# Optimization experiments

Measured on AMD Instinct MI355X. Metric: run time of the kernel, lower is better.

The kernel has to match this reference:

```python
import math
import jax, jax.numpy as jnp
import numpy as np

B, FEAT, H, W = 4, 256, 48, 48
NH = 8
PE = 10            # pe_dim -> 3*PE = 30 positional channels
DK = FEAT // NH    # 32
DV = FEAT // NH    # 32
SCALE = 2.0 * math.pi
TEMPERATURE = 10000.0
BN_EPS = 1e-5


def pos_en_sine(h, w, num_pos_feats=PE):
    """3-axis sine positional encoding (y, x, and a constant 'o' axis) -> [3*PE, h, w]."""
    eps = 1e-6
    ones = jnp.ones((h, w), jnp.float32)
    y_embed = jnp.cumsum(ones, axis=0)
    x_embed = jnp.cumsum(ones, axis=1)
    y_embed = y_embed / (y_embed[-1:, :] + eps) * SCALE
    x_embed = x_embed / (x_embed[:, -1:] + eps) * SCALE
    o_embed = ones * SCALE  # third axis, constant when no explicit pos is given
    dim_t = jnp.arange(num_pos_feats, dtype=jnp.float32)
    dim_t = TEMPERATURE ** (2.0 * jnp.floor(dim_t / 2.0) / num_pos_feats)

    def enc(e):  # e: [h, w] -> [h, w, PE] interleaved sin/cos
        p = e[..., None] / dim_t
        return jnp.stack([jnp.sin(p[..., 0::2]), jnp.cos(p[..., 1::2])], axis=-1).reshape(h, w, num_pos_feats)

    pe = jnp.concatenate([enc(y_embed), enc(x_embed), enc(o_embed)], axis=-1)  # [h, w, 3*PE]
    return jnp.transpose(pe, (2, 0, 1))  # [3*PE, h, w]


def conv1x1(w, x):  # w: [out_c, in_c], x: [b, in_c, h, w]
    return jnp.einsum('oc,bchw->bohw', w, x)


def setup_inputs() -> dict:
    key = jax.random.key(0)
    ks = jax.random.split(key, 16)
    s = 0.02
    return {
        'q': jax.random.normal(ks[0], (B, FEAT, H, W), jnp.float32),
        'k': jax.random.normal(ks[1], (B, FEAT, H, W), jnp.float32),
        'v': jax.random.normal(ks[2], (B, FEAT, H, W), jnp.float32),
        'wq': jax.random.normal(ks[3], (NH * DK, FEAT + 3 * PE), jnp.float32) * s,
        'wk': jax.random.normal(ks[4], (NH * DK, FEAT + 3 * PE), jnp.float32) * s,
        'wv': jax.random.normal(ks[5], (NH * DV, FEAT), jnp.float32) * s,
        'wfc': jax.random.normal(ks[6], (FEAT, NH * DV), jnp.float32) * s,
        'w1': jax.random.normal(ks[7], (FEAT, FEAT), jnp.float32) * s,
        'b1': jnp.zeros((FEAT,), jnp.float32),
        'w2': jax.random.normal(ks[8], (FEAT, FEAT), jnp.float32) * s,
        'b2': jnp.zeros((FEAT,), jnp.float32),
        'gamma': jnp.ones((FEAT,), jnp.float32),
        'beta': jnp.zeros((FEAT,), jnp.float32),
    }


def reference(q, k, v, wq, wk, wv, wfc, w1, b1, w2, b2, gamma, beta):
    b, c, h, w = q.shape
    n = h * w
    pe = pos_en_sine(h, w)                                # [3*PE, h, w]
    peb = jnp.broadcast_to(pe[None], (b,) + pe.shape)
    qc = jnp.concatenate([q, peb], axis=1)                # [b, FEAT+30, h, w]
    kc = jnp.concatenate([k, peb], axis=1)
    # multi-head softmax attention over all spatial tokens
    Q = conv1x1(wq, qc).reshape(b, NH, DK, n)             # [b, nh, dk, n]
    K = conv1x1(wk, kc).reshape(b, NH, DK, n)
    V = conv1x1(wv, v).reshape(b, NH, DV, n)
    scores = jnp.einsum('bhdn,bhdm->bhnm', Q, K) / jnp.sqrt(jnp.float32(DK))
    attn = jax.nn.softmax(scores, axis=-1)                # [b, nh, n, n]
    O = jnp.einsum('bhnm,bhdm->bhdn', attn, V).reshape(b, NH * DV, h, w)
    O = conv1x1(wfc, O)                                   # [b, FEAT, h, w]
    # pointwise FFN + residual
    h1 = jax.nn.relu(conv1x1(w1, O) + b1[None, :, None, None])
    h2 = conv1x1(w2, h1) + b2[None, :, None, None]
    out = O + h2
    # BatchNorm2d (training mode: batch statistics over (b, h, w), biased var)
    mean = jnp.mean(out, axis=(0, 2, 3), keepdims=True)
    var = jnp.var(out, axis=(0, 2, 3), keepdims=True)
    out = (out - mean) / jnp.sqrt(var + BN_EPS)
    out = out * gamma[None, :, None, None] + beta[None, :, None, None]
    return out
```

## Files before the change

kernel.cpp:

```cpp
#include <hip/hip_runtime.h>
#include <hip/hip_bf16.h>

#define NTOK 2304

typedef short  short8  __attribute__((ext_vector_type(8)));
typedef unsigned short ushort8v __attribute__((ext_vector_type(8)));
typedef float  f32x4   __attribute__((ext_vector_type(4)));

static __device__ __forceinline__ unsigned short f2bfu(float f){
  __hip_bfloat16 h = __float2bfloat16(f);
  union { __hip_bfloat16 h; unsigned short u; } cv; cv.h = h; return cv.u;
}

static __device__ __forceinline__ void plane32(unsigned &a, unsigned &b){
  asm("v_permlane32_swap_b32 %0, %1" : "+v"(a), "+v"(b));
}
static __device__ __forceinline__ void plane16(unsigned &a, unsigned &b){
  asm("v_permlane16_swap_b32 %0, %1" : "+v"(a), "+v"(b));
}
static __device__ __forceinline__ short8 xpose_p(f32x4 sa, f32x4 sb){
  unsigned x0, x1, y0, y1;
  asm("v_cvt_pk_bf16_f32 %0, %1, %2" : "=v"(x0) : "v"(sa[0]), "v"(sa[1]));
  asm("v_cvt_pk_bf16_f32 %0, %1, %2" : "=v"(x1) : "v"(sa[2]), "v"(sa[3]));
  asm("v_cvt_pk_bf16_f32 %0, %1, %2" : "=v"(y0) : "v"(sb[0]), "v"(sb[1]));
  asm("v_cvt_pk_bf16_f32 %0, %1, %2" : "=v"(y1) : "v"(sb[2]), "v"(sb[3]));
  plane32(x0, y0);
  plane32(x1, y1);
  plane16(x0, y0);
  plane16(x1, y1);
  union { unsigned u[4]; short8 s; } r;
  r.u[0] = x0; r.u[1] = x1; r.u[2] = y0; r.u[3] = y1;
  return r.s;
}


__global__ void trip_kernel(float* out, int n){
  int i = blockIdx.x*256 + threadIdx.x;
  if (i < n) out[i] = 1000.0f;
}

__global__ __launch_bounds__(256) void setup_kernel(
    const float* __restrict__ q, const float* __restrict__ k,
    const float* __restrict__ v,
    const float* __restrict__ wq, const float* __restrict__ wk,
    const float* __restrict__ wv, const float* __restrict__ wfc,
    const float* __restrict__ w1, const float* __restrict__ w2,
    unsigned short* __restrict__ qT, unsigned short* __restrict__ kT,
    unsigned short* __restrict__ vT,
    unsigned short* __restrict__ wqp, unsigned short* __restrict__ wkp,
    unsigned short* __restrict__ wvb, unsigned short* __restrict__ wfcb,
    unsigned short* __restrict__ w1b, unsigned short* __restrict__ w2b,
    float* __restrict__ bns){
  const int bid = blockIdx.x;
  const int t = threadIdx.x;
  __shared__ __align__(16) unsigned short tile[64*72];

  if (bid < 1728){
    if (bid == 0){ bns[t] = 0.f; bns[256+t] = 0.f; }
    const int x = bid % 36, rem = bid / 36;
    const int y = rem % 4, z = rem / 4;
    const int tz = z >> 2, b = z & 3;
    const float* src = (tz==0) ? q : ((tz==1) ? k : v);
    unsigned short* dst = (tz==0) ? qT : ((tz==1) ? kT : vT);
    const int W = (tz==2) ? 256 : 288;
    const int n0 = x*64, c0 = y*64;
    const int jj = t & 7, cl = t >> 3;
    #pragma unroll
    for (int p=0; p<2; p++){
      int c = c0 + 32*p + cl;
      const float* s = src + (size_t)(b*256 + c)*NTOK + n0 + 8*jj;
      float4 f0 = *(const float4*)s;
      float4 f1 = *(const float4*)(s + 4);
      unsigned short* tr = tile + 32*p + cl;
      tr[(8*jj+0)*72] = f2bfu(f0.x); tr[(8*jj+1)*72] = f2bfu(f0.y);
      tr[(8*jj+2)*72] = f2bfu(f0.z); tr[(8*jj+3)*72] = f2bfu(f0.w);
      tr[(8*jj+4)*72] = f2bfu(f1.x); tr[(8*jj+5)*72] = f2bfu(f1.y);
      tr[(8*jj+6)*72] = f2bfu(f1.z); tr[(8*jj+7)*72] = f2bfu(f1.w);
    }
    __syncthreads();
    #pragma unroll
    for (int p=0; p<2; p++){
      int nl = 32*p + cl;
      ushort8v val = *(const ushort8v*)(tile + nl*72 + 8*jj);
      *(ushort8v*)(dst + (size_t)(b*2304 + n0 + nl)*W + c0 + 8*jj) = val;
    }
  } else if (bid < 1800){
    const int id2 = bid - 1728;
    const int x = id2 % 9, yy = id2 / 9;
    const int n = x*256 + t;
    unsigned short* buf = (yy < 4) ? qT : kT;
    const int b = yy & 3;
    const int i = n / 48, j = n - 48*i;
    const float k2pi = 6.283185307179586f;
    const float f = k2pi / 48.000001f;
    float ey = (float)(i+1) * f;
    float ex = (float)(j+1) * f;
    unsigned short u[32];
    #pragma unroll
    for (int p=0; p<10; p++){
      float inv = exp2f(-2.6575424759098898f * (float)(p >> 1));
      float vy = ey*inv, vx = ex*inv, vo = k2pi*inv;
      u[p]    = f2bfu((p&1) ? cosf(vy) : sinf(vy));
      u[10+p] = f2bfu((p&1) ? cosf(vx) : sinf(vx));
      u[20+p] = f2bfu((p&1) ? cosf(vo) : sinf(vo));
    }
    u[30] = 0; u[31] = 0;
    unsigned short* dst = buf + (size_t)(b*2304 + n)*288 + 256;
    #pragma unroll
    for (int m=0; m<4; m++) *(ushort8v*)(dst + 8*m) = *(const ushort8v*)(u + 8*m);
  } else if (bid < 2376){
    const int id3 = bid - 1800;
    const int x = id3 % 288, y = id3 / 288;
    const int idx = x*256 + t;
    const float* src = y ? wk : wq;
    unsigned short* dst = y ? wkp : wqp;
    const float scale = y ? 1.f : 0.25503486f;
    int row = idx / 288, col = idx - row*288;
    dst[idx] = (col < 286) ? f2bfu(src[row*286 + col] * scale) : (unsigned short)0;
  } else {
    const int id4 = bid - 2376;
    const int x = id4 % 256, y = id4 / 256;
    const int idx = x*256 + t;
    const float* src = (y==0)?wv:((y==1)?wfc:((y==2)?w1:w2));
    unsigned short* dst = (y==0)?wvb:((y==1)?wfcb:((y==2)?w1b:w2b));
    dst[idx] = f2bfu(src[idx]);
  }
}

template<int KSTEPS>
static __device__ __forceinline__ void gemm_core(
    const unsigned short* __restrict__ arow,
    const unsigned short* __restrict__ wrow, int wstride, f32x4* acc){
  #pragma unroll
  for (int kk=0; kk<KSTEPS; kk++){
    short8 af = *(const short8*)(arow + 32*kk);
    #pragma unroll
    for (int to=0; to<2; to++){
      short8 bf = *(const short8*)(wrow + (size_t)(16*to)*wstride + 32*kk);
      acc[to] = __builtin_amdgcn_mfma_f32_16x16x32_bf16(af, bf, acc[to], 0,0,0);
    }
  }
}

static __device__ __forceinline__ void epi_tok(
    const f32x4* acc, unsigned short* __restrict__ out_tok,
    int b, int tok, int n0, int lane, int quad, int cc,
    unsigned short* __restrict__ tlw){
  #pragma unroll
  for (int to=0; to<2; to++)
    #pragma unroll
    for (int r=0; r<4; r++)
      tlw[(4*quad + r)*40 + 16*to + cc] = f2bfu(acc[to][r]);
  const int row = lane & 15, ch = lane >> 4;
  ushort8v val = *(const ushort8v*)(tlw + row*40 + 8*ch);
  *(ushort8v*)(out_tok + (size_t)(b*2304 + tok + row)*256 + n0 + 8*ch) = val;
}

static __device__ __forceinline__ void epi_chan(
    const f32x4* acc, unsigned short* __restrict__ out_chan,
    int b, int tok, int n0, int quad, int cc){
  #pragma unroll
  for (int to=0; to<2; to++){
    ushort4 pk;
    pk.x = f2bfu(acc[to][0]); pk.y = f2bfu(acc[to][1]);
    pk.z = f2bfu(acc[to][2]); pk.w = f2bfu(acc[to][3]);
    *(ushort4*)(out_chan + (size_t)(b*256 + n0 + 16*to + cc)*NTOK + tok + 4*quad) = pk;
  }
}

__global__ __launch_bounds__(256) void qkv_kernel(
    const unsigned short* __restrict__ qT, const unsigned short* __restrict__ kT,
    const unsigned short* __restrict__ vT,
    const unsigned short* __restrict__ wqp, const unsigned short* __restrict__ wkp,
    const unsigned short* __restrict__ wvb,
    unsigned short* __restrict__ Qt, unsigned short* __restrict__ Kt,
    unsigned short* __restrict__ V2){
  const int t = threadIdx.x;
  const int w = t >> 6, lane = t & 63;
  const int quad = lane >> 4, cc = lane & 15;
  const int t0 = blockIdx.x*64, n0 = blockIdx.y*32;
  const int tz = blockIdx.z >> 2, b = blockIdx.z & 3;
  const int tok = t0 + 16*w;
  __shared__ __align__(16) unsigned short tl[4*16*40];
  unsigned short* tlw = tl + w*640;

  f32x4 acc[2];
  acc[0] = (f32x4){0.f,0.f,0.f,0.f}; acc[1] = acc[0];

  if (tz == 0){
    const unsigned short* arow = qT + (size_t)(b*2304 + tok + cc)*288 + 8*quad;
    const unsigned short* wrow = wqp + (size_t)(n0 + cc)*288 + 8*quad;
    gemm_core<9>(arow, wrow, 288, acc);
    epi_tok(acc, Qt, b, tok, n0, lane, quad, cc, tlw);
  } else if (tz == 1){
    const unsigned short* arow = kT + (size_t)(b*2304 + tok + cc)*288 + 8*quad;
    const unsigned short* wrow = wkp + (size_t)(n0 + cc)*288 + 8*quad;
    gemm_core<9>(arow, wrow, 288, acc);
    epi_tok(acc, Kt, b, tok, n0, lane, quad, cc, tlw);
  } else {
    const unsigned short* arow = vT + (size_t)(b*2304 + tok + cc)*256 + 8*quad;
    const unsigned short* wrow = wvb + (size_t)(n0 + cc)*256 + 8*quad;
    gemm_core<8>(arow, wrow, 256, acc);
    epi_chan(acc, V2, b, tok, n0, quad, cc);
  }
}

template<int EPI>
__global__ __launch_bounds__(256) void gemm2_kernel(
    const unsigned short* __restrict__ aT,
    const unsigned short* __restrict__ wgt,
    const float* __restrict__ bias,
    unsigned short* __restrict__ out_tok,
    unsigned short* __restrict__ out_chan,
    const unsigned short* __restrict__ resid,
    float* __restrict__ pre_out, float* __restrict__ bns, int relu){
  const int t = threadIdx.x;
  const int w = t >> 6, lane = t & 63;
  const int quad = lane >> 4, cc = lane & 15;
  const int t0 = blockIdx.x*64, n0 = blockIdx.y*32, b = blockIdx.z;
  const int tok = t0 + 16*w;
  __shared__ __align__(16) unsigned short tl[4*16*40];
  unsigned short* tlw = tl + w*640;

  const unsigned short* arow = aT + (size_t)(b*2304 + tok + cc)*256 + 8*quad;
  const unsigned short* wrow = wgt + (size_t)(n0 + cc)*256 + 8*quad;
  f32x4 acc[2];
  acc[0] = (f32x4){0.f,0.f,0.f,0.f}; acc[1] = acc[0];
  gemm_core<8>(arow, wrow, 256, acc);

  if (bias){
    #pragma unroll
    for (int to=0; to<2; to++){
      float bv = bias[n0 + 16*to + cc];
      #pragma unroll
      for (int r=0; r<4; r++) acc[to][r] += bv;
    }
  }
  if (relu){
    #pragma unroll
    for (int to=0; to<2; to++)
      #pragma unroll
      for (int r=0; r<4; r++) acc[to][r] = fmaxf(acc[to][r], 0.f);
  }

  if (EPI == 2){
    epi_chan(acc, out_chan, b, tok, n0, quad, cc);
    epi_tok(acc, out_tok, b, tok, n0, lane, quad, cc, tlw);
  }
  if (EPI == 0){
    epi_tok(acc, out_tok, b, tok, n0, lane, quad, cc, tlw);
  }
  if (EPI == 3){
    #pragma unroll
    for (int to=0; to<2; to++){
      size_t co = (size_t)(b*256 + n0 + 16*to + cc)*NTOK + tok + 4*quad;
      ushort4 rr = *(const ushort4*)(resid + co);
      float p0 = acc[to][0] + __uint_as_float((unsigned)rr.x << 16);
      float p1 = acc[to][1] + __uint_as_float((unsigned)rr.y << 16);
      float p2 = acc[to][2] + __uint_as_float((unsigned)rr.z << 16);
      float p3 = acc[to][3] + __uint_as_float((unsigned)rr.w << 16);
      *(float4*)(pre_out + co) = make_float4(p0,p1,p2,p3);
      float s1 = (p0+p1)+(p2+p3);
      float s2 = (p0*p0+p1*p1)+(p2*p2+p3*p3);
      s1 += __shfl_xor(s1, 16, 64); s1 += __shfl_xor(s1, 32, 64);
      s2 += __shfl_xor(s2, 16, 64); s2 += __shfl_xor(s2, 32, 64);
      if (quad == 0){
        atomicAdd(&bns[n0 + 16*to + cc],       s1);
        atomicAdd(&bns[256 + n0 + 16*to + cc], s2);
      }
    }
  }
}

__global__ __launch_bounds__(256) void attn_kernel(
    const unsigned short* __restrict__ Qt, const unsigned short* __restrict__ Kt,
    const unsigned short* __restrict__ V2, unsigned short* __restrict__ AO){
  const int t = threadIdx.x;
  const int w = t >> 6, lane = t & 63;
  const int quad = lane >> 4, cc = lane & 15;
  const int h = blockIdx.y, b = blockIdx.z;
  const int q0 = blockIdx.x*32;

  const unsigned short* qb = Qt + (size_t)(b*2304 + q0 + cc)*256 + h*32 + 8*quad;
  short8 qf0 = *(const short8*)(qb);
  short8 qf1 = *(const short8*)(qb + 16*256);

  const unsigned short* kb = Kt + (size_t)(b*2304 + cc)*256 + h*32 + 8*quad;
  const unsigned short* vb = V2 + (size_t)(b*256 + h*32 + cc)*NTOK + 8*quad;

  __shared__ __align__(16) unsigned short attn_lds[10240];

  f32x4 o00 = {0.f,0.f,0.f,0.f}, o10 = o00, o01 = o00, o11 = o00;
  float lsum0 = 0.f, lsum1 = 0.f;

  const int kstart = w*576, kend = kstart + 576;
  short8 kf0 = *(const short8*)(kb + (size_t)kstart*256);
  short8 kf1 = *(const short8*)(kb + (size_t)(kstart+16)*256);
  short8 vf0 = *(const short8*)(vb + kstart);
  short8 vf1 = *(const short8*)(vb + (size_t)16*NTOK + kstart);

  #pragma unroll 1
  for (int k0 = kstart; k0 < kend; k0 += 32){
    int kn = (k0 + 32 < kend) ? k0 + 32 : kstart;
    short8 nk0 = *(const short8*)(kb + (size_t)kn*256);
    short8 nk1 = *(const short8*)(kb + (size_t)(kn+16)*256);
    short8 nv0 = *(const short8*)(vb + kn);
    short8 nv1 = *(const short8*)(vb + (size_t)16*NTOK + kn);

    f32x4 z = {0.f,0.f,0.f,0.f};
    f32x4 s00 = __builtin_amdgcn_mfma_f32_16x16x32_bf16(kf0, qf0, z, 0,0,0);
    f32x4 s10 = __builtin_amdgcn_mfma_f32_16x16x32_bf16(kf1, qf0, z, 0,0,0);
    f32x4 s01 = __builtin_amdgcn_mfma_f32_16x16x32_bf16(kf0, qf1, z, 0,0,0);
    f32x4 s11 = __builtin_amdgcn_mfma_f32_16x16x32_bf16(kf1, qf1, z, 0,0,0);

    #pragma unroll
    for (int r=0; r<4; r++){
      s00[r] = __builtin_amdgcn_exp2f(s00[r]);
      s10[r] = __builtin_amdgcn_exp2f(s10[r]);
      s01[r] = __builtin_amdgcn_exp2f(s01[r]);
      s11[r] = __builtin_amdgcn_exp2f(s11[r]);
    }
    lsum0 += ((s00[0]+s00[1])+(s00[2]+s00[3])) + ((s10[0]+s10[1])+(s10[2]+s10[3]));
    lsum1 += ((s01[0]+s01[1])+(s01[2]+s01[3])) + ((s11[0]+s11[1])+(s11[2]+s11[3]));

    short8 pf0 = xpose_p(s00, s10);
    short8 pf1 = xpose_p(s01, s11);

    o00 = __builtin_amdgcn_mfma_f32_16x16x32_bf16(vf0, pf0, o00, 0,0,0);
    o10 = __builtin_amdgcn_mfma_f32_16x16x32_bf16(vf1, pf0, o10, 0,0,0);
    o01 = __builtin_amdgcn_mfma_f32_16x16x32_bf16(vf0, pf1, o01, 0,0,0);
    o11 = __builtin_amdgcn_mfma_f32_16x16x32_bf16(vf1, pf1, o11, 0,0,0);

    kf0 = nk0; kf1 = nk1; vf0 = nv0; vf1 = nv1;
  }

  lsum0 += __shfl_xor(lsum0, 16, 64); lsum0 += __shfl_xor(lsum0, 32, 64);
  lsum1 += __shfl_xor(lsum1, 16, 64); lsum1 += __shfl_xor(lsum1, 32, 64);

  float* mg = (float*)(attn_lds + w*2560);
  {
    const int base = lane*17;
    #pragma unroll
    for (int i=0;i<4;i++){
      mg[base + i]      = o00[i];
      mg[base + 4 + i]  = o10[i];
      mg[base + 8 + i]  = o01[i];
      mg[base + 12 + i] = o11[i];
    }
    mg[1088 + lane] = lsum0;
    mg[1152 + lane] = lsum1;
  }
  __syncthreads();

  const float* m0 = (const float*)(attn_lds);
  const float* m1 = (const float*)(attn_lds + 2560);
  const float* m2 = (const float*)(attn_lds + 5120);
  const float* m3 = (const float*)(attn_lds + 7680);
  float ls0 = (m0[1088+lane]+m1[1088+lane]) + (m2[1088+lane]+m3[1088+lane]);
  float ls1 = (m0[1152+lane]+m1[1152+lane]) + (m2[1152+lane]+m3[1152+lane]);
  float inv = 1.f / ((w & 2) ? ls1 : ls0);

  const int off = lane*17 + w*4;
  float r0 = (m0[off+0]+m1[off+0]) + (m2[off+0]+m3[off+0]);
  float r1 = (m0[off+1]+m1[off+1]) + (m2[off+1]+m3[off+1]);
  float r2 = (m0[off+2]+m1[off+2]) + (m2[off+2]+m3[off+2]);
  float r3 = (m0[off+3]+m1[off+3]) + (m2[off+3]+m3[off+3]);

  const int qcol = q0 + ((w & 2) ? 16 : 0) + cc;
  const int dofs = (w & 1) ? 16 : 0;
  ushort4 pk;
  pk.x = f2bfu(r0*inv); pk.y = f2bfu(r1*inv);
  pk.z = f2bfu(r2*inv); pk.w = f2bfu(r3*inv);
  *(ushort4*)(AO + (size_t)(b*2304 + qcol)*256 + h*32 + dofs + 4*quad) = pk;
}

__global__ __launch_bounds__(256) void bn_final_kernel(
    const float* __restrict__ pre, const float* __restrict__ bns,
    const float* __restrict__ g, const float* __restrict__ bt,
    float* __restrict__ out){
  int i0 = (blockIdx.x*256 + threadIdx.x)*4;
  int ch = (i0 / NTOK) & 255;
  float mean = bns[ch] * (1.f/9216.f);
  float var  = bns[256+ch] * (1.f/9216.f) - mean*mean;
  float scl = g[ch] * rsqrtf(fmaxf(var, 0.f) + 1e-5f);
  float sh  = bt[ch] - mean*scl;
  float4 x = *(const float4*)(pre + i0);
  *(float4*)(out + i0) = make_float4(x.x*scl+sh, x.y*scl+sh, x.z*scl+sh, x.w*scl+sh);
}

extern "C" void kernel_launch(void* const* d_in, const int* in_sizes, int n_in,
                              void* d_out, int out_size, void* d_ws, size_t ws_size,
                              hipStream_t stream){
  const size_t NEED = 2112 + (size_t)15155200*2;
  if (ws_size < NEED){
    trip_kernel<<<dim3((out_size+255)/256), dim3(256), 0, stream>>>((float*)d_out, out_size);
    return;
  }
  const float* q   = (const float*)d_in[0];
  const float* k   = (const float*)d_in[1];
  const float* v   = (const float*)d_in[2];
  const float* wq  = (const float*)d_in[3];
  const float* wk  = (const float*)d_in[4];
  const float* wv  = (const float*)d_in[5];
  const float* wfc = (const float*)d_in[6];
  const float* w1  = (const float*)d_in[7];
  const float* b1  = (const float*)d_in[8];
  const float* w2  = (const float*)d_in[9];
  const float* b2  = (const float*)d_in[10];
  const float* gm  = (const float*)d_in[11];
  const float* bt  = (const float*)d_in[12];

  float* ws  = (float*)d_ws;
  float* bns = ws;
  unsigned short* ub = (unsigned short*)(ws + 528);
  unsigned short* u_qT = ub;
  unsigned short* u_kT = ub + 2654208;
  unsigned short* u_vT = ub + 5308416;
  unsigned short* u_Qt = ub + 7667712;
  unsigned short* u_Kt = ub + 10027008;
  unsigned short* u_V2 = ub + 12386304;
  unsigned short* wqp  = ub + 14745600;
  unsigned short* wkp  = ub + 14819328;
  unsigned short* wvb  = ub + 14893056;
  unsigned short* wfcb = ub + 14958592;
  unsigned short* w1b  = ub + 15024128;
  unsigned short* w2b  = ub + 15089664;
  unsigned short* AO  = u_qT;
  unsigned short* h1  = u_kT;
  unsigned short* Ofc = u_vT;
  unsigned short* Oc  = u_Qt;
  float* pre = (float*)(u_Kt);

  setup_kernel<<<dim3(3400), dim3(256), 0, stream>>>(
      q, k, v, wq, wk, wv, wfc, w1, w2,
      u_qT, u_kT, u_vT, wqp, wkp, wvb, wfcb, w1b, w2b, bns);

  qkv_kernel<<<dim3(36,8,12), dim3(256), 0, stream>>>(u_qT, u_kT, u_vT, wqp, wkp, wvb, u_Qt, u_Kt, u_V2);

  attn_kernel<<<dim3(72,8,4), dim3(256), 0, stream>>>(u_Qt, u_Kt, u_V2, AO);

  gemm2_kernel<2><<<dim3(36,8,4), dim3(256), 0, stream>>>(AO,  wfcb, nullptr, Ofc, Oc, nullptr, nullptr, nullptr, 0);
  gemm2_kernel<0><<<dim3(36,8,4), dim3(256), 0, stream>>>(Ofc, w1b,  b1,      h1,  nullptr, nullptr, nullptr, nullptr, 1);
  gemm2_kernel<3><<<dim3(36,8,4), dim3(256), 0, stream>>>(h1,  w2b,  b2,      nullptr, nullptr, Oc, pre, bns, 0);

  bn_final_kernel<<<dim3(2304), dim3(256), 0, stream>>>(pre, bns, gm, bt, (float*)d_out);
}
```

Measured before the change: 268.2 us.

## Remap attention blocks to XCDs and double the K/V tile per loop step

The attention grid becomes a flat 1D launch. Block indices are remapped so that each XCD (chosen by index mod 8) handles four whole (batch, head) groups, which is meant to keep K/V reuse inside one XCD's L2 cache. The inner key loop now processes 64 keys per iteration as two 32-key halves and prefetches both halves of the next step. This gives the scheduler more independent MFMA and exp work to overlap with global loads, at the cost of higher register pressure. The 576 keys per wave divide evenly into 64-key steps, so correctness holds.

```diff
diff --git a/kernel.cpp b/kernel.cpp
--- a/kernel.cpp
+++ b/kernel.cpp
@@ -278,8 +278,15 @@
   const int t = threadIdx.x;
   const int w = t >> 6, lane = t & 63;
   const int quad = lane >> 4, cc = lane & 15;
-  const int h = blockIdx.y, b = blockIdx.z;
-  const int q0 = blockIdx.x*32;
+
+  const int flat = blockIdx.x;
+  const int xcd = flat & 7;
+  const int ii  = flat >> 3;
+  const int sub = ii / 72;
+  const int g   = xcd*4 + sub;
+  const int qblk = ii - sub*72;
+  const int h = g & 7, b = g >> 3;
+  const int q0 = qblk*32;
 
   const unsigned short* qb = Qt + (size_t)(b*2304 + q0 + cc)*256 + h*32 + 8*quad;
   short8 qf0 = *(const short8*)(qb);
@@ -294,44 +301,71 @@
   float lsum0 = 0.f, lsum1 = 0.f;
 
   const int kstart = w*576, kend = kstart + 576;
-  short8 kf0 = *(const short8*)(kb + (size_t)kstart*256);
-  short8 kf1 = *(const short8*)(kb + (size_t)(kstart+16)*256);
-  short8 vf0 = *(const short8*)(vb + kstart);
-  short8 vf1 = *(const short8*)(vb + (size_t)16*NTOK + kstart);
+  short8 ka0 = *(const short8*)(kb + (size_t)kstart*256);
+  short8 ka1 = *(const short8*)(kb + (size_t)(kstart+16)*256);
+  short8 va0 = *(const short8*)(vb + kstart);
+  short8 va1 = *(const short8*)(vb + (size_t)16*NTOK + kstart);
+  short8 kb0 = *(const short8*)(kb + (size_t)(kstart+32)*256);
+  short8 kb1 = *(const short8*)(kb + (size_t)(kstart+48)*256);
+  short8 vb0 = *(const short8*)(vb + kstart + 32);
+  short8 vb1 = *(const short8*)(vb + (size_t)16*NTOK + kstart + 32);
 
   #pragma unroll 1
-  for (int k0 = kstart; k0 < kend; k0 += 32){
-    int kn = (k0 + 32 < kend) ? k0 + 32 : kstart;
-    short8 nk0 = *(const short8*)(kb + (size_t)kn*256);
-    short8 nk1 = *(const short8*)(kb + (size_t)(kn+16)*256);
-    short8 nv0 = *(const short8*)(vb + kn);
-    short8 nv1 = *(const short8*)(vb + (size_t)16*NTOK + kn);
+  for (int k0 = kstart; k0 < kend; k0 += 64){
+    int kn = (k0 + 64 < kend) ? k0 + 64 : kstart;
+    short8 na0 = *(const short8*)(kb + (size_t)kn*256);
+    short8 na1 = *(const short8*)(kb + (size_t)(kn+16)*256);
+    short8 wa0 = *(const short8*)(vb + kn);
+    short8 wa1 = *(const short8*)(vb + (size_t)16*NTOK + kn);
+    short8 nb0 = *(const short8*)(kb + (size_t)(kn+32)*256);
+    short8 nb1 = *(const short8*)(kb + (size_t)(kn+48)*256);
+    short8 wb0 = *(const short8*)(vb + kn + 32);
+    short8 wb1 = *(const short8*)(vb + (size_t)16*NTOK + kn + 32);
 
     f32x4 z = {0.f,0.f,0.f,0.f};
-    f32x4 s00 = __builtin_amdgcn_mfma_f32_16x16x32_bf16(kf0, qf0, z, 0,0,0);
-    f32x4 s10 = __builtin_amdgcn_mfma_f32_16x16x32_bf16(kf1, qf0, z, 0,0,0);
-    f32x4 s01 = __builtin_amdgcn_mfma_f32_16x16x32_bf16(kf0, qf1, z, 0,0,0);
-    f32x4 s11 = __builtin_amdgcn_mfma_f32_16x16x32_bf16(kf1, qf1, z, 0,0,0);
+    f32x4 sA00 = __builtin_amdgcn_mfma_f32_16x16x32_bf16(ka0, qf0, z, 0,0,0);
+    f32x4 sA10 = __builtin_amdgcn_mfma_f32_16x16x32_bf16(ka1, qf0, z, 0,0,0);
+    f32x4 sA01 = __builtin_amdgcn_mfma_f32_16x16x32_bf16(ka0, qf1, z, 0,0,0);
+    f32x4 sA11 = __builtin_amdgcn_mfma_f32_16x16x32_bf16(ka1, qf1, z, 0,0,0);
+    f32x4 sB00 = __builtin_amdgcn_mfma_f32_16x16x32_bf16(kb0, qf0, z, 0,0,0);
+    f32x4 sB10 = __builtin_amdgcn_mfma_f32_16x16x32_bf16(kb1, qf0, z, 0,0,0);
+    f32x4 sB01 = __builtin_amdgcn_mfma_f32_16x16x32_bf16(kb0, qf1, z, 0,0,0);
+    f32x4 sB11 = __builtin_amdgcn_mfma_f32_16x16x32_bf16(kb1, qf1, z, 0,0,0);
 
     #pragma unroll
     for (int r=0; r<4; r++){
-      s00[r] = __builtin_amdgcn_exp2f(s00[r]);
-      s10[r] = __builtin_amdgcn_exp2f(s10[r]);
-      s01[r] = __builtin_amdgcn_exp2f(s01[r]);
-      s11[r] = __builtin_amdgcn_exp2f(s11[r]);
-    }
-    lsum0 += ((s00[0]+s00[1])+(s00[2]+s00[3])) + ((s10[0]+s10[1])+(s10[2]+s10[3]));
-    lsum1 += ((s01[0]+s01[1])+(s01[2]+s01[3])) + ((s11[0]+s11[1])+(s11[2]+s11[3]));
-
-    short8 pf0 = xpose_p(s00, s10);
-    short8 pf1 = xpose_p(s01, s11);
-
-    o00 = __builtin_amdgcn_mfma_f32_16x16x32_bf16(vf0, pf0, o00, 0,0,0);
-    o10 = __builtin_amdgcn_mfma_f32_16x16x32_bf16(vf1, pf0, o10, 0,0,0);
-    o01 = __builtin_amdgcn_mfma_f32_16x16x32_bf16(vf0, pf1, o01, 0,0,0);
-    o11 = __builtin_amdgcn_mfma_f32_16x16x32_bf16(vf1, pf1, o11, 0,0,0);
-
-    kf0 = nk0; kf1 = nk1; vf0 = nv0; vf1 = nv1;
+      sA00[r] = __builtin_amdgcn_exp2f(sA00[r]);
+      sA10[r] = __builtin_amdgcn_exp2f(sA10[r]);
+      sA01[r] = __builtin_amdgcn_exp2f(sA01[r]);
+      sA11[r] = __builtin_amdgcn_exp2f(sA11[r]);
+    }
+    lsum0 += ((sA00[0]+sA00[1])+(sA00[2]+sA00[3])) + ((sA10[0]+sA10[1])+(sA10[2]+sA10[3]));
+    lsum1 += ((sA01[0]+sA01[1])+(sA01[2]+sA01[3])) + ((sA11[0]+sA11[1])+(sA11[2]+sA11[3]));
+    short8 pfA0 = xpose_p(sA00, sA10);
+    short8 pfA1 = xpose_p(sA01, sA11);
+    o00 = __builtin_amdgcn_mfma_f32_16x16x32_bf16(va0, pfA0, o00, 0,0,0);
+    o10 = __builtin_amdgcn_mfma_f32_16x16x32_bf16(va1, pfA0, o10, 0,0,0);
+    o01 = __builtin_amdgcn_mfma_f32_16x16x32_bf16(va0, pfA1, o01, 0,0,0);
+    o11 = __builtin_amdgcn_mfma_f32_16x16x32_bf16(va1, pfA1, o11, 0,0,0);
+
+    #pragma unroll
+    for (int r=0; r<4; r++){
+      sB00[r] = __builtin_amdgcn_exp2f(sB00[r]);
+      sB10[r] = __builtin_amdgcn_exp2f(sB10[r]);
+      sB01[r] = __builtin_amdgcn_exp2f(sB01[r]);
+      sB11[r] = __builtin_amdgcn_exp2f(sB11[r]);
+    }
+    lsum0 += ((sB00[0]+sB00[1])+(sB00[2]+sB00[3])) + ((sB10[0]+sB10[1])+(sB10[2]+sB10[3]));
+    lsum1 += ((sB01[0]+sB01[1])+(sB01[2]+sB01[3])) + ((sB11[0]+sB11[1])+(sB11[2]+sB11[3]));
+    short8 pfB0 = xpose_p(sB00, sB10);
+    short8 pfB1 = xpose_p(sB01, sB11);
+    o00 = __builtin_amdgcn_mfma_f32_16x16x32_bf16(vb0, pfB0, o00, 0,0,0);
+    o10 = __builtin_amdgcn_mfma_f32_16x16x32_bf16(vb1, pfB0, o10, 0,0,0);
+    o01 = __builtin_amdgcn_mfma_f32_16x16x32_bf16(vb0, pfB1, o01, 0,0,0);
+    o11 = __builtin_amdgcn_mfma_f32_16x16x32_bf16(vb1, pfB1, o11, 0,0,0);
+
+    ka0 = na0; ka1 = na1; va0 = wa0; va1 = wa1;
+    kb0 = nb0; kb1 = nb1; vb0 = wb0; vb1 = wb1;
   }
 
   lsum0 += __shfl_xor(lsum0, 16, 64); lsum0 += __shfl_xor(lsum0, 32, 64);
@@ -437,7 +471,7 @@
 
   qkv_kernel<<<dim3(36,8,12), dim3(256), 0, stream>>>(u_qT, u_kT, u_vT, wqp, wkp, wvb, u_Qt, u_Kt, u_V2);
 
-  attn_kernel<<<dim3(72,8,4), dim3(256), 0, stream>>>(u_Qt, u_Kt, u_V2, AO);
+  attn_kernel<<<dim3(2304), dim3(256), 0, stream>>>(u_Qt, u_Kt, u_V2, AO);
 
   gemm2_kernel<2><<<dim3(36,8,4), dim3(256), 0, stream>>>(AO,  wfcb, nullptr, Ofc, Oc, nullptr, nullptr, nullptr, 0);
   gemm2_kernel<0><<<dim3(36,8,4), dim3(256), 0, stream>>>(Ofc, w1b,  b1,      h1,  nullptr, nullptr, nullptr, nullptr, 1);
```

Measured after the change: 282.1 us. +5.2%, slower.

## Remap attention grid per XCD, two heads per block, double-buffer K/V

Applied to the files above, without the earlier changes.

The attention kernel now launches a flat grid whose block index is decoded so that all query tiles of one (batch, head-pair) group land on the same XCD, which should improve L2 reuse of K and V. Each block handles two heads: each pair of waves shares a head and splits the 2304 keys in half, instead of four waves splitting one head's keys. The key loop is unrolled by two with separate A and B register buffers, so more K/V loads are in flight while the MFMA and exp work runs. The LDS merge now reduces two partials per head instead of four. The cost is more live registers per wave, which could lower occupancy.

```diff
diff --git a/kernel.cpp b/kernel.cpp
--- a/kernel.cpp
+++ b/kernel.cpp
@@ -278,8 +278,16 @@
   const int t = threadIdx.x;
   const int w = t >> 6, lane = t & 63;
   const int quad = lane >> 4, cc = lane & 15;
-  const int h = blockIdx.y, b = blockIdx.z;
-  const int q0 = blockIdx.x*32;
+
+  const int flat = blockIdx.x;
+  const int xcd = flat & 7;
+  const int ii  = flat >> 3;
+  const int sub = ii / 72;
+  const int g   = xcd*2 + sub;
+  const int qblk = ii - sub*72;
+  const int b = g >> 2, hp = g & 3;
+  const int h = hp*2 + (w >> 1);
+  const int q0 = qblk*32;
 
   const unsigned short* qb = Qt + (size_t)(b*2304 + q0 + cc)*256 + h*32 + 8*quad;
   short8 qf0 = *(const short8*)(qb);
@@ -293,26 +301,30 @@
   f32x4 o00 = {0.f,0.f,0.f,0.f}, o10 = o00, o01 = o00, o11 = o00;
   float lsum0 = 0.f, lsum1 = 0.f;
 
-  const int kstart = w*576, kend = kstart + 576;
-  short8 kf0 = *(const short8*)(kb + (size_t)kstart*256);
-  short8 kf1 = *(const short8*)(kb + (size_t)(kstart+16)*256);
-  short8 vf0 = *(const short8*)(vb + kstart);
-  short8 vf1 = *(const short8*)(vb + (size_t)16*NTOK + kstart);
+  const int kstart = (w & 1)*1152;
+  short8 kA0 = *(const short8*)(kb + (size_t)kstart*256);
+  short8 kA1 = *(const short8*)(kb + (size_t)(kstart+16)*256);
+  short8 vA0 = *(const short8*)(vb + kstart);
+  short8 vA1 = *(const short8*)(vb + (size_t)16*NTOK + kstart);
+  short8 kB0 = *(const short8*)(kb + (size_t)(kstart+32)*256);
+  short8 kB1 = *(const short8*)(kb + (size_t)(kstart+48)*256);
+  short8 vB0 = *(const short8*)(vb + kstart + 32);
+  short8 vB1 = *(const short8*)(vb + (size_t)16*NTOK + kstart + 32);
 
   #pragma unroll 1
-  for (int k0 = kstart; k0 < kend; k0 += 32){
-    int kn = (k0 + 32 < kend) ? k0 + 32 : kstart;
-    short8 nk0 = *(const short8*)(kb + (size_t)kn*256);
-    short8 nk1 = *(const short8*)(kb + (size_t)(kn+16)*256);
-    short8 nv0 = *(const short8*)(vb + kn);
-    short8 nv1 = *(const short8*)(vb + (size_t)16*NTOK + kn);
-
+  for (int it = 0; it < 18; ++it){
+    const int ko = kstart + it*64;
     f32x4 z = {0.f,0.f,0.f,0.f};
-    f32x4 s00 = __builtin_amdgcn_mfma_f32_16x16x32_bf16(kf0, qf0, z, 0,0,0);
-    f32x4 s10 = __builtin_amdgcn_mfma_f32_16x16x32_bf16(kf1, qf0, z, 0,0,0);
-    f32x4 s01 = __builtin_amdgcn_mfma_f32_16x16x32_bf16(kf0, qf1, z, 0,0,0);
-    f32x4 s11 = __builtin_amdgcn_mfma_f32_16x16x32_bf16(kf1, qf1, z, 0,0,0);
-
+
+    f32x4 s00 = __builtin_amdgcn_mfma_f32_16x16x32_bf16(kA0, qf0, z, 0,0,0);
+    f32x4 s10 = __builtin_amdgcn_mfma_f32_16x16x32_bf16(kA1, qf0, z, 0,0,0);
+    f32x4 s01 = __builtin_amdgcn_mfma_f32_16x16x32_bf16(kA0, qf1, z, 0,0,0);
+    f32x4 s11 = __builtin_amdgcn_mfma_f32_16x16x32_bf16(kA1, qf1, z, 0,0,0);
+    {
+      const int ra = (it < 17) ? ko + 64 : kstart;
+      kA0 = *(const short8*)(kb + (size_t)ra*256);
+      kA1 = *(const short8*)(kb + (size_t)(ra+16)*256);
+    }
     #pragma unroll
     for (int r=0; r<4; r++){
       s00[r] = __builtin_amdgcn_exp2f(s00[r]);
@@ -322,16 +334,51 @@
     }
     lsum0 += ((s00[0]+s00[1])+(s00[2]+s00[3])) + ((s10[0]+s10[1])+(s10[2]+s10[3]));
     lsum1 += ((s01[0]+s01[1])+(s01[2]+s01[3])) + ((s11[0]+s11[1])+(s11[2]+s11[3]));
-
-    short8 pf0 = xpose_p(s00, s10);
-    short8 pf1 = xpose_p(s01, s11);
-
-    o00 = __builtin_amdgcn_mfma_f32_16x16x32_bf16(vf0, pf0, o00, 0,0,0);
-    o10 = __builtin_amdgcn_mfma_f32_16x16x32_bf16(vf1, pf0, o10, 0,0,0);
-    o01 = __builtin_amdgcn_mfma_f32_16x16x32_bf16(vf0, pf1, o01, 0,0,0);
-    o11 = __builtin_amdgcn_mfma_f32_16x16x32_bf16(vf1, pf1, o11, 0,0,0);
-
-    kf0 = nk0; kf1 = nk1; vf0 = nv0; vf1 = nv1;
+    {
+      short8 pf0 = xpose_p(s00, s10);
+      short8 pf1 = xpose_p(s01, s11);
+      o00 = __builtin_amdgcn_mfma_f32_16x16x32_bf16(vA0, pf0, o00, 0,0,0);
+      o10 = __builtin_amdgcn_mfma_f32_16x16x32_bf16(vA1, pf0, o10, 0,0,0);
+      o01 = __builtin_amdgcn_mfma_f32_16x16x32_bf16(vA0, pf1, o01, 0,0,0);
+      o11 = __builtin_amdgcn_mfma_f32_16x16x32_bf16(vA1, pf1, o11, 0,0,0);
+    }
+    {
+      const int ra = (it < 17) ? ko + 64 : kstart;
+      vA0 = *(const short8*)(vb + ra);
+      vA1 = *(const short8*)(vb + (size_t)16*NTOK + ra);
+    }
+
+    f32x4 u00 = __builtin_amdgcn_mfma_f32_16x16x32_bf16(kB0, qf0, z, 0,0,0);
+    f32x4 u10 = __builtin_amdgcn_mfma_f32_16x16x32_bf16(kB1, qf0, z, 0,0,0);
+    f32x4 u01 = __builtin_amdgcn_mfma_f32_16x16x32_bf16(kB0, qf1, z, 0,0,0);
+    f32x4 u11 = __builtin_amdgcn_mfma_f32_16x16x32_bf16(kB1, qf1, z, 0,0,0);
+    {
+      const int rb = (it < 17) ? ko + 96 : kstart + 32;
+      kB0 = *(const short8*)(kb + (size_t)rb*256);
+      kB1 = *(const short8*)(kb + (size_t)(rb+16)*256);
+    }
+    #pragma unroll
+    for (int r=0; r<4; r++){
+      u00[r] = __builtin_amdgcn_exp2f(u00[r]);
+      u10[r] = __builtin_amdgcn_exp2f(u10[r]);
+      u01[r] = __builtin_amdgcn_exp2f(u01[r]);
+      u11[r] = __builtin_amdgcn_exp2f(u11[r]);
+    }
+    lsum0 += ((u00[0]+u00[1])+(u00[2]+u00[3])) + ((u10[0]+u10[1])+(u10[2]+u10[3]));
+    lsum1 += ((u01[0]+u01[1])+(u01[2]+u01[3])) + ((u11[0]+u11[1])+(u11[2]+u11[3]));
+    {
+      short8 pf0 = xpose_p(u00, u10);
+      short8 pf1 = xpose_p(u01, u11);
+      o00 = __builtin_amdgcn_mfma_f32_16x16x32_bf16(vB0, pf0, o00, 0,0,0);
+      o10 = __builtin_amdgcn_mfma_f32_16x16x32_bf16(vB1, pf0, o10, 0,0,0);
+      o01 = __builtin_amdgcn_mfma_f32_16x16x32_bf16(vB0, pf1, o01, 0,0,0);
+      o11 = __builtin_amdgcn_mfma_f32_16x16x32_bf16(vB1, pf1, o11, 0,0,0);
+    }
+    {
+      const int rb = (it < 17) ? ko + 96 : kstart + 32;
+      vB0 = *(const short8*)(vb + rb);
+      vB1 = *(const short8*)(vb + (size_t)16*NTOK + rb);
+    }
   }
 
   lsum0 += __shfl_xor(lsum0, 16, 64); lsum0 += __shfl_xor(lsum0, 32, 64);
@@ -352,26 +399,32 @@
   }
   __syncthreads();
 
-  const float* m0 = (const float*)(attn_lds);
-  const float* m1 = (const float*)(attn_lds + 2560);
-  const float* m2 = (const float*)(attn_lds + 5120);
-  const float* m3 = (const float*)(attn_lds + 7680);
-  float ls0 = (m0[1088+lane]+m1[1088+lane]) + (m2[1088+lane]+m3[1088+lane]);
-  float ls1 = (m0[1152+lane]+m1[1152+lane]) + (m2[1152+lane]+m3[1152+lane]);
-  float inv = 1.f / ((w & 2) ? ls1 : ls0);
-
-  const int off = lane*17 + w*4;
-  float r0 = (m0[off+0]+m1[off+0]) + (m2[off+0]+m3[off+0]);
-  float r1 = (m0[off+1]+m1[off+1]) + (m2[off+1]+m3[off+1]);
-  float r2 = (m0[off+2]+m1[off+2]) + (m2[off+2]+m3[off+2]);
-  float r3 = (m0[off+3]+m1[off+3]) + (m2[off+3]+m3[off+3]);
-
-  const int qcol = q0 + ((w & 2) ? 16 : 0) + cc;
-  const int dofs = (w & 1) ? 16 : 0;
-  ushort4 pk;
-  pk.x = f2bfu(r0*inv); pk.y = f2bfu(r1*inv);
-  pk.z = f2bfu(r2*inv); pk.w = f2bfu(r3*inv);
-  *(ushort4*)(AO + (size_t)(b*2304 + qcol)*256 + h*32 + dofs + 4*quad) = pk;
+  const float* mA = (const float*)(attn_lds + (w >> 1)*5120);
+  const float* mB = (const float*)(attn_lds + (w >> 1)*5120 + 2560);
+  const int tsel = w & 1;
+  float ls = tsel ? (mA[1152+lane]+mB[1152+lane]) : (mA[1088+lane]+mB[1088+lane]);
+  float inv = 1.f / ls;
+
+  const int off = lane*17 + tsel*8;
+  float r0 = mA[off+0]+mB[off+0];
+  float r1 = mA[off+1]+mB[off+1];
+  float r2 = mA[off+2]+mB[off+2];
+  float r3 = mA[off+3]+mB[off+3];
+  float r4 = mA[off+4]+mB[off+4];
+  float r5 = mA[off+5]+mB[off+5];
+  float r6 = mA[off+6]+mB[off+6];
+  float r7 = mA[off+7]+mB[off+7];
+
+  const int qcol = q0 + tsel*16 + cc;
+  unsigned short* dst = AO + (size_t)(b*2304 + qcol)*256 + h*32 + 4*quad;
+  ushort4 p0;
+  p0.x = f2bfu(r0*inv); p0.y = f2bfu(r1*inv);
+  p0.z = f2bfu(r2*inv); p0.w = f2bfu(r3*inv);
+  *(ushort4*)(dst) = p0;
+  ushort4 p1;
+  p1.x = f2bfu(r4*inv); p1.y = f2bfu(r5*inv);
+  p1.z = f2bfu(r6*inv); p1.w = f2bfu(r7*inv);
+  *(ushort4*)(dst + 16) = p1;
 }
 
 __global__ __launch_bounds__(256) void bn_final_kernel(
@@ -437,7 +490,7 @@
 
   qkv_kernel<<<dim3(36,8,12), dim3(256), 0, stream>>>(u_qT, u_kT, u_vT, wqp, wkp, wvb, u_Qt, u_Kt, u_V2);
 
-  attn_kernel<<<dim3(72,8,4), dim3(256), 0, stream>>>(u_Qt, u_Kt, u_V2, AO);
+  attn_kernel<<<dim3(1152), dim3(256), 0, stream>>>(u_Qt, u_Kt, u_V2, AO);
 
   gemm2_kernel<2><<<dim3(36,8,4), dim3(256), 0, stream>>>(AO,  wfcb, nullptr, Ofc, Oc, nullptr, nullptr, nullptr, 0);
   gemm2_kernel<0><<<dim3(36,8,4), dim3(256), 0, stream>>>(Ofc, w1b,  b1,      h1,  nullptr, nullptr, nullptr, nullptr, 1);
```

Result: slower. 278.6 us (+3.9%).

## Process 64 queries per attention block to reuse K/V fragments across more queries

Applied to the files above, without the earlier changes.

Each attention block now handles 64 queries instead of 32, so each loaded K and V fragment feeds twice as many MFMAs and total K/V global traffic is halved. The grid shrinks from 72 to 36 blocks along the query axis. The cross-wave merge in LDS moves to a column-major layout, and each wave now writes 16 queries across all 32 head dims. The next-tile K/V loads are issued right after the MFMAs that consume the current ones instead of at the top of the loop. The cost is higher register pressure and fewer blocks (1152), which may reduce occupancy and latency hiding.

```diff
diff --git a/kernel.cpp b/kernel.cpp
--- a/kernel.cpp
+++ b/kernel.cpp
@@ -279,39 +279,45 @@
   const int w = t >> 6, lane = t & 63;
   const int quad = lane >> 4, cc = lane & 15;
   const int h = blockIdx.y, b = blockIdx.z;
-  const int q0 = blockIdx.x*32;
+  const int q0 = blockIdx.x*64;
 
   const unsigned short* qb = Qt + (size_t)(b*2304 + q0 + cc)*256 + h*32 + 8*quad;
   short8 qf0 = *(const short8*)(qb);
   short8 qf1 = *(const short8*)(qb + 16*256);
+  short8 qf2 = *(const short8*)(qb + 32*256);
+  short8 qf3 = *(const short8*)(qb + 48*256);
 
   const unsigned short* kb = Kt + (size_t)(b*2304 + cc)*256 + h*32 + 8*quad;
   const unsigned short* vb = V2 + (size_t)(b*256 + h*32 + cc)*NTOK + 8*quad;
 
-  __shared__ __align__(16) unsigned short attn_lds[10240];
-
-  f32x4 o00 = {0.f,0.f,0.f,0.f}, o10 = o00, o01 = o00, o11 = o00;
-  float lsum0 = 0.f, lsum1 = 0.f;
-
-  const int kstart = w*576, kend = kstart + 576;
+  __shared__ __align__(16) float mg_lds[4*2112];
+
+  f32x4 o00={0.f,0.f,0.f,0.f}, o10=o00, o01=o00, o11=o00;
+  f32x4 o02=o00, o12=o00, o03=o00, o13=o00;
+  float lsum0=0.f, lsum1=0.f, lsum2=0.f, lsum3=0.f;
+
+  const int kstart = w*576;
   short8 kf0 = *(const short8*)(kb + (size_t)kstart*256);
   short8 kf1 = *(const short8*)(kb + (size_t)(kstart+16)*256);
   short8 vf0 = *(const short8*)(vb + kstart);
   short8 vf1 = *(const short8*)(vb + (size_t)16*NTOK + kstart);
 
   #pragma unroll 1
-  for (int k0 = kstart; k0 < kend; k0 += 32){
-    int kn = (k0 + 32 < kend) ? k0 + 32 : kstart;
-    short8 nk0 = *(const short8*)(kb + (size_t)kn*256);
-    short8 nk1 = *(const short8*)(kb + (size_t)(kn+16)*256);
-    short8 nv0 = *(const short8*)(vb + kn);
-    short8 nv1 = *(const short8*)(vb + (size_t)16*NTOK + kn);
-
-    f32x4 z = {0.f,0.f,0.f,0.f};
+  for (int it = 0; it < 18; ++it){
+    const int ko = kstart + it*32;
+    const int rk = (it < 17) ? ko + 32 : kstart;
+    const f32x4 z = {0.f,0.f,0.f,0.f};
+
     f32x4 s00 = __builtin_amdgcn_mfma_f32_16x16x32_bf16(kf0, qf0, z, 0,0,0);
     f32x4 s10 = __builtin_amdgcn_mfma_f32_16x16x32_bf16(kf1, qf0, z, 0,0,0);
     f32x4 s01 = __builtin_amdgcn_mfma_f32_16x16x32_bf16(kf0, qf1, z, 0,0,0);
     f32x4 s11 = __builtin_amdgcn_mfma_f32_16x16x32_bf16(kf1, qf1, z, 0,0,0);
+    f32x4 s02 = __builtin_amdgcn_mfma_f32_16x16x32_bf16(kf0, qf2, z, 0,0,0);
+    f32x4 s12 = __builtin_amdgcn_mfma_f32_16x16x32_bf16(kf1, qf2, z, 0,0,0);
+    f32x4 s03 = __builtin_amdgcn_mfma_f32_16x16x32_bf16(kf0, qf3, z, 0,0,0);
+    f32x4 s13 = __builtin_amdgcn_mfma_f32_16x16x32_bf16(kf1, qf3, z, 0,0,0);
+    kf0 = *(const short8*)(kb + (size_t)rk*256);
+    kf1 = *(const short8*)(kb + (size_t)(rk+16)*256);
 
     #pragma unroll
     for (int r=0; r<4; r++){
@@ -319,59 +325,96 @@
       s10[r] = __builtin_amdgcn_exp2f(s10[r]);
       s01[r] = __builtin_amdgcn_exp2f(s01[r]);
       s11[r] = __builtin_amdgcn_exp2f(s11[r]);
+      s02[r] = __builtin_amdgcn_exp2f(s02[r]);
+      s12[r] = __builtin_amdgcn_exp2f(s12[r]);
+      s03[r] = __builtin_amdgcn_exp2f(s03[r]);
+      s13[r] = __builtin_amdgcn_exp2f(s13[r]);
     }
     lsum0 += ((s00[0]+s00[1])+(s00[2]+s00[3])) + ((s10[0]+s10[1])+(s10[2]+s10[3]));
     lsum1 += ((s01[0]+s01[1])+(s01[2]+s01[3])) + ((s11[0]+s11[1])+(s11[2]+s11[3]));
+    lsum2 += ((s02[0]+s02[1])+(s02[2]+s02[3])) + ((s12[0]+s12[1])+(s12[2]+s12[3]));
+    lsum3 += ((s03[0]+s03[1])+(s03[2]+s03[3])) + ((s13[0]+s13[1])+(s13[2]+s13[3]));
 
     short8 pf0 = xpose_p(s00, s10);
     short8 pf1 = xpose_p(s01, s11);
+    short8 pf2 = xpose_p(s02, s12);
+    short8 pf3 = xpose_p(s03, s13);
 
     o00 = __builtin_amdgcn_mfma_f32_16x16x32_bf16(vf0, pf0, o00, 0,0,0);
     o10 = __builtin_amdgcn_mfma_f32_16x16x32_bf16(vf1, pf0, o10, 0,0,0);
     o01 = __builtin_amdgcn_mfma_f32_16x16x32_bf16(vf0, pf1, o01, 0,0,0);
     o11 = __builtin_amdgcn_mfma_f32_16x16x32_bf16(vf1, pf1, o11, 0,0,0);
-
-    kf0 = nk0; kf1 = nk1; vf0 = nv0; vf1 = nv1;
+    o02 = __builtin_amdgcn_mfma_f32_16x16x32_bf16(vf0, pf2, o02, 0,0,0);
+    o12 = __builtin_amdgcn_mfma_f32_16x16x32_bf16(vf1, pf2, o12, 0,0,0);
+    o03 = __builtin_amdgcn_mfma_f32_16x16x32_bf16(vf0, pf3, o03, 0,0,0);
+    o13 = __builtin_amdgcn_mfma_f32_16x16x32_bf16(vf1, pf3, o13, 0,0,0);
+    vf0 = *(const short8*)(vb + rk);
+    vf1 = *(const short8*)(vb + (size_t)16*NTOK + rk);
   }
 
   lsum0 += __shfl_xor(lsum0, 16, 64); lsum0 += __shfl_xor(lsum0, 32, 64);
   lsum1 += __shfl_xor(lsum1, 16, 64); lsum1 += __shfl_xor(lsum1, 32, 64);
-
-  float* mg = (float*)(attn_lds + w*2560);
+  lsum2 += __shfl_xor(lsum2, 16, 64); lsum2 += __shfl_xor(lsum2, 32, 64);
+  lsum3 += __shfl_xor(lsum3, 16, 64); lsum3 += __shfl_xor(lsum3, 32, 64);
+
+  float* mg = mg_lds + w*2112;
+  #pragma unroll
+  for (int i=0;i<4;i++){
+    mg[(0*8 + 0*4 + i)*64 + lane] = o00[i];
+    mg[(0*8 + 1*4 + i)*64 + lane] = o10[i];
+    mg[(1*8 + 0*4 + i)*64 + lane] = o01[i];
+    mg[(1*8 + 1*4 + i)*64 + lane] = o11[i];
+    mg[(2*8 + 0*4 + i)*64 + lane] = o02[i];
+    mg[(2*8 + 1*4 + i)*64 + lane] = o12[i];
+    mg[(3*8 + 0*4 + i)*64 + lane] = o03[i];
+    mg[(3*8 + 1*4 + i)*64 + lane] = o13[i];
+  }
+  if (quad == 0){
+    mg[2048 +  0 + cc] = lsum0;
+    mg[2048 + 16 + cc] = lsum1;
+    mg[2048 + 32 + cc] = lsum2;
+    mg[2048 + 48 + cc] = lsum3;
+  }
+  __syncthreads();
+
+  const float* m0 = mg_lds;
+  const float* m1 = mg_lds + 2112;
+  const float* m2 = mg_lds + 4224;
+  const float* m3 = mg_lds + 6336;
+  const int la = 2048 + w*16 + cc;
+  float ls = (m0[la] + m1[la]) + (m2[la] + m3[la]);
+  float inv = 1.f / ls;
+
+  float r0, r1, r2, r3, r4, r5, r6, r7;
   {
-    const int base = lane*17;
-    #pragma unroll
-    for (int i=0;i<4;i++){
-      mg[base + i]      = o00[i];
-      mg[base + 4 + i]  = o10[i];
-      mg[base + 8 + i]  = o01[i];
-      mg[base + 12 + i] = o11[i];
-    }
-    mg[1088 + lane] = lsum0;
-    mg[1152 + lane] = lsum1;
-  }
-  __syncthreads();
-
-  const float* m0 = (const float*)(attn_lds);
-  const float* m1 = (const float*)(attn_lds + 2560);
-  const float* m2 = (const float*)(attn_lds + 5120);
-  const float* m3 = (const float*)(attn_lds + 7680);
-  float ls0 = (m0[1088+lane]+m1[1088+lane]) + (m2[1088+lane]+m3[1088+lane]);
-  float ls1 = (m0[1152+lane]+m1[1152+lane]) + (m2[1152+lane]+m3[1152+lane]);
-  float inv = 1.f / ((w & 2) ? ls1 : ls0);
-
-  const int off = lane*17 + w*4;
-  float r0 = (m0[off+0]+m1[off+0]) + (m2[off+0]+m3[off+0]);
-  float r1 = (m0[off+1]+m1[off+1]) + (m2[off+1]+m3[off+1]);
-  float r2 = (m0[off+2]+m1[off+2]) + (m2[off+2]+m3[off+2]);
-  float r3 = (m0[off+3]+m1[off+3]) + (m2[off+3]+m3[off+3]);
-
-  const int qcol = q0 + ((w & 2) ? 16 : 0) + cc;
-  const int dofs = (w & 1) ? 16 : 0;
-  ushort4 pk;
-  pk.x = f2bfu(r0*inv); pk.y = f2bfu(r1*inv);
-  pk.z = f2bfu(r2*inv); pk.w = f2bfu(r3*inv);
-  *(ushort4*)(AO + (size_t)(b*2304 + qcol)*256 + h*32 + dofs + 4*quad) = pk;
+    int a0 = (w*8 + 0)*64 + lane;
+    r0 = (m0[a0] + m1[a0]) + (m2[a0] + m3[a0]);
+    int a1 = (w*8 + 1)*64 + lane;
+    r1 = (m0[a1] + m1[a1]) + (m2[a1] + m3[a1]);
+    int a2 = (w*8 + 2)*64 + lane;
+    r2 = (m0[a2] + m1[a2]) + (m2[a2] + m3[a2]);
+    int a3 = (w*8 + 3)*64 + lane;
+    r3 = (m0[a3] + m1[a3]) + (m2[a3] + m3[a3]);
+    int a4 = (w*8 + 4)*64 + lane;
+    r4 = (m0[a4] + m1[a4]) + (m2[a4] + m3[a4]);
+    int a5 = (w*8 + 5)*64 + lane;
+    r5 = (m0[a5] + m1[a5]) + (m2[a5] + m3[a5]);
+    int a6 = (w*8 + 6)*64 + lane;
+    r6 = (m0[a6] + m1[a6]) + (m2[a6] + m3[a6]);
+    int a7 = (w*8 + 7)*64 + lane;
+    r7 = (m0[a7] + m1[a7]) + (m2[a7] + m3[a7]);
+  }
+
+  const int qcol = q0 + w*16 + cc;
+  unsigned short* dst = AO + (size_t)(b*2304 + qcol)*256 + h*32 + 4*quad;
+  ushort4 p0;
+  p0.x = f2bfu(r0*inv); p0.y = f2bfu(r1*inv);
+  p0.z = f2bfu(r2*inv); p0.w = f2bfu(r3*inv);
+  *(ushort4*)(dst) = p0;
+  ushort4 p1;
+  p1.x = f2bfu(r4*inv); p1.y = f2bfu(r5*inv);
+  p1.z = f2bfu(r6*inv); p1.w = f2bfu(r7*inv);
+  *(ushort4*)(dst + 16) = p1;
 }
 
 __global__ __launch_bounds__(256) void bn_final_kernel(
@@ -437,7 +480,7 @@
 
   qkv_kernel<<<dim3(36,8,12), dim3(256), 0, stream>>>(u_qT, u_kT, u_vT, wqp, wkp, wvb, u_Qt, u_Kt, u_V2);
 
-  attn_kernel<<<dim3(72,8,4), dim3(256), 0, stream>>>(u_Qt, u_Kt, u_V2, AO);
+  attn_kernel<<<dim3(36,8,4), dim3(256), 0, stream>>>(u_Qt, u_Kt, u_V2, AO);
 
   gemm2_kernel<2><<<dim3(36,8,4), dim3(256), 0, stream>>>(AO,  wfcb, nullptr, Ofc, Oc, nullptr, nullptr, nullptr, 0);
   gemm2_kernel<0><<<dim3(36,8,4), dim3(256), 0, stream>>>(Ofc, w1b,  b1,      h1,  nullptr, nullptr, nullptr, nullptr, 1);
```

New measurement: 248.4 us. 7.4% less time.
